# Kernel tuning notes

Measured on AMD Instinct MI355X. Metric: run time of the kernel, lower is better.

Reference implementation:

```python
import jax, jax.numpy as jnp
import numpy as np

N, D = 32768, 512
MARGIN = 1.0


def setup_inputs() -> dict:
    key = jax.random.key(0)
    k1, k2, k3, k4 = jax.random.split(key, 4)
    image_outputs = jax.random.normal(k1, (N, D), dtype=jnp.float32)
    audio_outputs = jax.random.normal(k2, (N, D), dtype=jnp.float32)
    ar = jnp.arange(N, dtype=jnp.int32)
    # impostor indices, guaranteed != i (matches the while-loop resampling intent)
    I_imp = jax.random.randint(k3, (N,), 0, N, dtype=jnp.int32)
    I_imp = jnp.where(I_imp == ar, (I_imp + 1) % N, I_imp)
    A_imp = jax.random.randint(k4, (N,), 0, N, dtype=jnp.int32)
    A_imp = jnp.where(A_imp == ar, (A_imp + 1) % N, A_imp)
    return {
        "image_outputs": image_outputs,
        "audio_outputs": audio_outputs,
        "I_imp_ind": I_imp,
        "A_imp_ind": A_imp,
    }


def reference(image_outputs, audio_outputs, I_imp_ind, A_imp_ind):
    # per-row dot products; [n]
    anchorsim = jnp.sum(image_outputs * audio_outputs, axis=-1)
    Iimpsim = jnp.sum(image_outputs[I_imp_ind] * audio_outputs, axis=-1)
    Aimpsim = jnp.sum(image_outputs * audio_outputs[A_imp_ind], axis=-1)
    # `if (simdif > 0): loss += simdif` == hinge (relu)
    a2i = jax.nn.relu(MARGIN + Iimpsim - anchorsim)
    i2a = jax.nn.relu(MARGIN + Aimpsim - anchorsim)
    n = image_outputs.shape[0]
    return jnp.sum(a2i + i2a) / n
```

## Files before the change

### kernel.cpp

```cpp
#include <hip/hip_runtime.h>

#define NROWS  32768
#define DDIM   512
#define BLOCKS 2048

__global__ __launch_bounds__(256) void dotloss_main(
    const float* __restrict__ img,
    const float* __restrict__ aud,
    const int*   __restrict__ iimp,
    const int*   __restrict__ aimp,
    float* __restrict__ partial)
{
    const int tid = threadIdx.x;
    const int g   = tid & 15;
    const int grp = tid >> 4;
    const int row = (blockIdx.x << 4) + grp;

    const int ii = iimp[row];
    const int ai = aimp[row];

    const float4* __restrict__ imR = (const float4*)(img + (size_t)row * DDIM) + g;
    const float4* __restrict__ auR = (const float4*)(aud + (size_t)row * DDIM) + g;
    const float4* __restrict__ imI = (const float4*)(img + (size_t)ii  * DDIM) + g;
    const float4* __restrict__ auA = (const float4*)(aud + (size_t)ai  * DDIM) + g;

    float u = 0.f, v = 0.f;

    #pragma unroll
    for (int k = 0; k < 8; ++k) {
        float4 a = imR[16 * k];
        float4 b = auR[16 * k];
        float4 c = imI[16 * k];
        float4 d = auA[16 * k];
        u += (c.x - a.x) * b.x + (c.y - a.y) * b.y
           + (c.z - a.z) * b.z + (c.w - a.w) * b.w;
        v += a.x * (d.x - b.x) + a.y * (d.y - b.y)
           + a.z * (d.z - b.z) + a.w * (d.w - b.w);
    }

    #pragma unroll
    for (int off = 1; off < 16; off <<= 1) {
        u += __shfl_xor(u, off, 64);
        v += __shfl_xor(v, off, 64);
    }

    float loss = fmaxf(0.f, 1.f + u) + fmaxf(0.f, 1.f + v);

    __shared__ float s[16];
    if (g == 0) s[grp] = loss;
    __syncthreads();
    if (tid == 0) {
        float t = 0.f;
        #pragma unroll
        for (int i = 0; i < 16; ++i) t += s[i];
        partial[blockIdx.x] = t;
    }
}

__global__ __launch_bounds__(256) void dotloss_reduce(
    const float* __restrict__ partial,
    float* __restrict__ out)
{
    const int tid = threadIdx.x;
    float t = 0.f;
    #pragma unroll
    for (int k = 0; k < BLOCKS / 256; ++k) t += partial[tid + 256 * k];

    #pragma unroll
    for (int off = 32; off > 0; off >>= 1) t += __shfl_xor(t, off, 64);

    __shared__ float s[4];
    if ((tid & 63) == 0) s[tid >> 6] = t;
    __syncthreads();
    if (tid == 0) out[0] = (s[0] + s[1] + s[2] + s[3]) * (1.0f / (float)NROWS);
}

extern "C" void kernel_launch(void* const* d_in, const int* in_sizes, int n_in,
                              void* d_out, int out_size, void* d_ws, size_t ws_size,
                              hipStream_t stream) {
    const float* img  = (const float*)d_in[0];
    const float* aud  = (const float*)d_in[1];
    const int*   iimp = (const int*)d_in[2];
    const int*   aimp = (const int*)d_in[3];
    float* out     = (float*)d_out;
    float* partial = (float*)d_ws;

    dotloss_main<<<BLOCKS, 256, 0, stream>>>(img, aud, iimp, aimp, partial);
    dotloss_reduce<<<1, 256, 0, stream>>>(partial, out);
}
```

Before: 42.79 us.

## Assign one wave per row with eight rows per wave and double-buffered loads

The main kernel now uses one 64-lane wave per row instead of 16 threads per row. Each wave handles eight consecutive rows, with a two-buffer software pipeline that issues the next row's loads before reducing the current one. The grid shrinks to 512 blocks of 512 threads, and the reduce kernel reads 512 partials. This aims to keep more memory requests in flight per wave and cut block count, at the cost of more registers, a full-wave shuffle reduction per row, and fewer waves available to hide latency.

```diff
diff --git a/kernel.cpp b/kernel.cpp
--- a/kernel.cpp
+++ b/kernel.cpp
@@ -1,58 +1,92 @@
 #include <hip/hip_runtime.h>
 
-#define NROWS  32768
-#define DDIM   512
-#define BLOCKS 2048
+#define NROWS 32768
+#define DDIM  512
+#define NF4   (DDIM / 4)
+#define WGS   512
+#define TPB   512
+#define RPW   8
 
-__global__ __launch_bounds__(256) void dotloss_main(
+struct RowBuf { float4 A0, A1, B0, B1, C0, C1, D0, D1; };
+
+__device__ __forceinline__ void load_row(RowBuf& R,
+    const float4* __restrict__ ibase, const float4* __restrict__ abase,
+    int row, int ii, int ai, int lane)
+{
+    const float4* pR = ibase + (size_t)row * NF4 + lane;
+    const float4* qR = abase + (size_t)row * NF4 + lane;
+    const float4* pI = ibase + (size_t)ii  * NF4 + lane;
+    const float4* qA = abase + (size_t)ai  * NF4 + lane;
+    R.A0 = pR[0]; R.A1 = pR[64];
+    R.B0 = qR[0]; R.B1 = qR[64];
+    R.C0 = pI[0]; R.C1 = pI[64];
+    R.D0 = qA[0]; R.D1 = qA[64];
+}
+
+__device__ __forceinline__ float row_loss(const RowBuf& R)
+{
+    float u = (R.C0.x - R.A0.x) * R.B0.x + (R.C0.y - R.A0.y) * R.B0.y
+            + (R.C0.z - R.A0.z) * R.B0.z + (R.C0.w - R.A0.w) * R.B0.w
+            + (R.C1.x - R.A1.x) * R.B1.x + (R.C1.y - R.A1.y) * R.B1.y
+            + (R.C1.z - R.A1.z) * R.B1.z + (R.C1.w - R.A1.w) * R.B1.w;
+    float v = R.A0.x * (R.D0.x - R.B0.x) + R.A0.y * (R.D0.y - R.B0.y)
+            + R.A0.z * (R.D0.z - R.B0.z) + R.A0.w * (R.D0.w - R.B0.w)
+            + R.A1.x * (R.D1.x - R.B1.x) + R.A1.y * (R.D1.y - R.B1.y)
+            + R.A1.z * (R.D1.z - R.B1.z) + R.A1.w * (R.D1.w - R.B1.w);
+    #pragma unroll
+    for (int off = 1; off < 64; off <<= 1) {
+        u += __shfl_xor(u, off, 64);
+        v += __shfl_xor(v, off, 64);
+    }
+    return fmaxf(0.f, 1.f + u) + fmaxf(0.f, 1.f + v);
+}
+
+__global__ __launch_bounds__(TPB, 4) void dotloss_main(
     const float* __restrict__ img,
     const float* __restrict__ aud,
     const int*   __restrict__ iimp,
     const int*   __restrict__ aimp,
     float* __restrict__ partial)
 {
-    const int tid = threadIdx.x;
-    const int g   = tid & 15;
-    const int grp = tid >> 4;
-    const int row = (blockIdx.x << 4) + grp;
+    const int lane = threadIdx.x & 63;
+    const int wave = threadIdx.x >> 6;
+    const int gw   = (blockIdx.x << 3) + wave;
+    const int row0 = gw * RPW;
 
-    const int ii = iimp[row];
-    const int ai = aimp[row];
+    const float4* ibase = (const float4*)img;
+    const float4* abase = (const float4*)aud;
 
-    const float4* __restrict__ imR = (const float4*)(img + (size_t)row * DDIM) + g;
-    const float4* __restrict__ auR = (const float4*)(aud + (size_t)row * DDIM) + g;
-    const float4* __restrict__ imI = (const float4*)(img + (size_t)ii  * DDIM) + g;
-    const float4* __restrict__ auA = (const float4*)(aud + (size_t)ai  * DDIM) + g;
+    RowBuf X, Y;
+    float acc = 0.f;
 
-    float u = 0.f, v = 0.f;
-
-    #pragma unroll
-    for (int k = 0; k < 8; ++k) {
-        float4 a = imR[16 * k];
-        float4 b = auR[16 * k];
-        float4 c = imI[16 * k];
-        float4 d = auA[16 * k];
-        u += (c.x - a.x) * b.x + (c.y - a.y) * b.y
-           + (c.z - a.z) * b.z + (c.w - a.w) * b.w;
-        v += a.x * (d.x - b.x) + a.y * (d.y - b.y)
-           + a.z * (d.z - b.z) + a.w * (d.w - b.w);
+    {
+        int ii = iimp[row0], ai = aimp[row0];
+        load_row(X, ibase, abase, row0, ii, ai, lane);
     }
 
     #pragma unroll
-    for (int off = 1; off < 16; off <<= 1) {
-        u += __shfl_xor(u, off, 64);
-        v += __shfl_xor(v, off, 64);
+    for (int r = 0; r < RPW; r += 2) {
+        {
+            int r1 = row0 + r + 1;
+            int i1 = iimp[r1], a1 = aimp[r1];
+            load_row(Y, ibase, abase, r1, i1, a1, lane);
+        }
+        acc += row_loss(X);
+        if (r + 2 < RPW) {
+            int r2 = row0 + r + 2;
+            int i2 = iimp[r2], a2 = aimp[r2];
+            load_row(X, ibase, abase, r2, i2, a2, lane);
+        }
+        acc += row_loss(Y);
     }
 
-    float loss = fmaxf(0.f, 1.f + u) + fmaxf(0.f, 1.f + v);
-
-    __shared__ float s[16];
-    if (g == 0) s[grp] = loss;
+    __shared__ float s[TPB / 64];
+    if (lane == 0) s[wave] = acc;
     __syncthreads();
-    if (tid == 0) {
+    if (threadIdx.x == 0) {
         float t = 0.f;
         #pragma unroll
-        for (int i = 0; i < 16; ++i) t += s[i];
+        for (int w = 0; w < TPB / 64; ++w) t += s[w];
         partial[blockIdx.x] = t;
     }
 }
@@ -62,9 +96,7 @@
     float* __restrict__ out)
 {
     const int tid = threadIdx.x;
-    float t = 0.f;
-    #pragma unroll
-    for (int k = 0; k < BLOCKS / 256; ++k) t += partial[tid + 256 * k];
+    float t = partial[tid] + partial[tid + 256];
 
     #pragma unroll
     for (int off = 32; off > 0; off >>= 1) t += __shfl_xor(t, off, 64);
@@ -85,6 +117,6 @@
     float* out     = (float*)d_out;
     float* partial = (float*)d_ws;
 
-    dotloss_main<<<BLOCKS, 256, 0, stream>>>(img, aud, iimp, aimp, partial);
+    dotloss_main<<<WGS, TPB, 0, stream>>>(img, aud, iimp, aimp, partial);
     dotloss_reduce<<<1, 256, 0, stream>>>(partial, out);
 }
```

Result: slower. 46.83 us (+9.5%).
